# Kernel optimization log

Hardware: AMD Instinct MI355X
Metric: run time of the kernel (lower is better)

The kernel has to match this reference:

```python
import jax, jax.numpy as jnp
import numpy as np

B, S, D = 8, 1024, 1024
H, DH = 16, 64  # n_heads, d_head; D == H*DH


def setup_inputs() -> dict:
    key = jax.random.key(0)
    ks = jax.random.split(key, 7)
    scale = 1.0 / np.sqrt(DH)
    return {
        "images": jax.random.normal(ks[0], (B, S, D), dtype=jnp.float32),
        "Wq": jax.random.normal(ks[1], (H, DH, DH), dtype=jnp.float32) * scale,
        "bq": jax.random.normal(ks[2], (H, DH), dtype=jnp.float32) * scale,
        "Wk": jax.random.normal(ks[3], (H, DH, DH), dtype=jnp.float32) * scale,
        "bk": jax.random.normal(ks[4], (H, DH), dtype=jnp.float32) * scale,
        "Wv": jax.random.normal(ks[5], (H, DH, DH), dtype=jnp.float32) * scale,
        "bv": jax.random.normal(ks[6], (H, DH), dtype=jnp.float32) * scale,
    }


def reference(images, Wq, bq, Wk, bk, Wv, bv):
    Bn, Sn, Dn = images.shape
    x = images.reshape(Bn, Sn, H, DH)  # split hidden dim into per-head slices
    # torch Linear: y = x @ W.T + b, per head -> einsum over input dim d
    q = jnp.einsum("bshd,hod->bsho", x, Wq) + bq  # [B,S,H,DH]
    k = jnp.einsum("bshd,hod->bsho", x, Wk) + bk
    v = jnp.einsum("bshd,hod->bsho", x, Wv) + bv
    scores = jnp.einsum("bqhd,bkhd->bhqk", q, k) / jnp.sqrt(jnp.asarray(DH, x.dtype))
    attn = jax.nn.softmax(scores, axis=-1)  # [B,H,S,S]
    out = jnp.einsum("bhqk,bkhd->bqhd", attn, v)  # [B,S,H,DH]
    return out.reshape(Bn, Sn, Dn)  # hstack across heads == reshape back
```

## Files before the change

kernel.cpp:

```cpp
#include <hip/hip_runtime.h>
#include <hip/hip_bf16.h>

#define B_ 8
#define S_ 1024
#define D_ 1024
#define H_ 16
#define DH_ 64

typedef __attribute__((ext_vector_type(8))) short short8;
typedef __attribute__((ext_vector_type(8))) unsigned short ushort8;
typedef __attribute__((ext_vector_type(4))) unsigned short us4;
typedef __attribute__((ext_vector_type(4))) unsigned int uint4v;
typedef __attribute__((ext_vector_type(4))) float f32x4;

#define QSCALE 0.18033688011112042f

static __device__ __forceinline__ unsigned short f2bf(float f) {
    union { float f; unsigned u; } v; v.f = f;
    unsigned r = v.u + 0x7fffu + ((v.u >> 16) & 1u);
    return (unsigned short)(r >> 16);
}

static __device__ __forceinline__ void stage8(const float* __restrict__ src, unsigned short* dst) {
    float4 a = *reinterpret_cast<const float4*>(src);
    float4 b = *reinterpret_cast<const float4*>(src + 4);
    ushort8 r;
    r[0] = f2bf(a.x); r[1] = f2bf(a.y); r[2] = f2bf(a.z); r[3] = f2bf(a.w);
    r[4] = f2bf(b.x); r[5] = f2bf(b.y); r[6] = f2bf(b.z); r[7] = f2bf(b.w);
    *reinterpret_cast<ushort8*>(dst) = r;
}

static __device__ __forceinline__ unsigned int cvtpk(float a, float b) {
    unsigned int r;
    asm("v_cvt_pk_bf16_f32 %0, %1, %2" : "=v"(r) : "v"(a), "v"(b));
    return r;
}

__global__ __launch_bounds__(256) void qkv_proj(
    const float* __restrict__ x,
    const float* __restrict__ Wq, const float* __restrict__ bq,
    const float* __restrict__ Wk, const float* __restrict__ bk,
    const float* __restrict__ Wv, const float* __restrict__ bv,
    unsigned short* __restrict__ qo, unsigned short* __restrict__ ko,
    unsigned short* __restrict__ vo)
{
    const int bid   = blockIdx.x;
    const int stile = bid & 15;
    const int h     = (bid >> 4) & (H_ - 1);
    const int b     = bid >> 8;
    const int tid   = threadIdx.x;
    const int lane  = tid & 63;
    const int wave  = tid >> 6;
    const int lr    = lane & 15;
    const int lk    = lane >> 4;

    __shared__ __align__(16) unsigned short xs[64][72];
    __shared__ __align__(16) unsigned short wsh[3][64][72];

    {
        int row = tid >> 2;
        int col = (tid & 3) * 16;
        const float* src = x + ((size_t)(b * S_ + stile * 64 + row)) * D_ + h * DH_ + col;
        stage8(src,     &xs[row][col]);
        stage8(src + 8, &xs[row][col + 8]);
        const float* wsrc[3] = { Wq + h * DH_ * DH_, Wk + h * DH_ * DH_, Wv + h * DH_ * DH_ };
        #pragma unroll
        for (int p = 0; p < 3; ++p) {
            const float* s = wsrc[p] + row * DH_ + col;
            stage8(s,     &wsh[p][row][col]);
            stage8(s + 8, &wsh[p][row][col + 8]);
        }
    }
    __syncthreads();

    short8 a[2];
    #pragma unroll
    for (int kk = 0; kk < 2; ++kk)
        a[kk] = *reinterpret_cast<const short8*>(&xs[wave * 16 + lr][8 * lk + 32 * kk]);

    f32x4 acc[3][4];
    #pragma unroll
    for (int p = 0; p < 3; ++p)
        #pragma unroll
        for (int n = 0; n < 4; ++n)
            acc[p][n] = (f32x4){0.f, 0.f, 0.f, 0.f};

    #pragma unroll
    for (int p = 0; p < 3; ++p)
        #pragma unroll
        for (int kk = 0; kk < 2; ++kk)
            #pragma unroll
            for (int n = 0; n < 4; ++n) {
                short8 bf = *reinterpret_cast<const short8*>(&wsh[p][lr + 16 * n][8 * lk + 32 * kk]);
                acc[p][n] = __builtin_amdgcn_mfma_f32_16x16x32_bf16(a[kk], bf, acc[p][n], 0, 0, 0);
            }

    size_t base = ((size_t)(b * H_ + h) * S_ + stile * 64 + wave * 16) * DH_;
    #pragma unroll
    for (int p = 0; p < 2; ++p) {
        const float* bias = p ? (bk + h * DH_) : (bq + h * DH_);
        unsigned short* op = p ? ko : qo;
        #pragma unroll
        for (int n = 0; n < 4; ++n) {
            int col = lr + 16 * n;
            float bb = bias[col];
            #pragma unroll
            for (int r = 0; r < 4; ++r) {
                float val = acc[p][n][r] + bb;
                if (p == 0) val *= QSCALE;
                op[base + (size_t)(4 * lk + r) * DH_ + col] = f2bf(val);
            }
        }
    }
    {
        size_t vbase = (size_t)(b * H_ + h) * DH_ * S_;
        int s0 = stile * 64 + wave * 16 + 4 * lk;
        #pragma unroll
        for (int n = 0; n < 4; ++n) {
            int dh = lr + 16 * n;
            float bb = bv[h * DH_ + dh];
            us4 w;
            #pragma unroll
            for (int r = 0; r < 4; ++r) w[r] = f2bf(acc[2][n][r] + bb);
            *reinterpret_cast<us4*>(vo + vbase + (size_t)dh * S_ + s0) = w;
        }
    }
}

__global__ __launch_bounds__(256, 4) void attn_fwd(
    const unsigned short* __restrict__ q,
    const unsigned short* __restrict__ k,
    const unsigned short* __restrict__ vt,
    float* __restrict__ out)
{
    const int bid   = (blockIdx.x & 7) * 256 + (blockIdx.x >> 3);
    const int qtile = bid & 15;
    const int h     = (bid >> 4) & (H_ - 1);
    const int b     = bid >> 8;
    const int tid   = threadIdx.x;
    const int lane  = tid & 63;
    const int wave  = tid >> 6;
    const int lr    = lane & 15;
    const int lk    = lane >> 4;

    __shared__ __align__(16) unsigned short ks[2][64][72];
    __shared__ __align__(16) unsigned short vs[2][64][72];

    const size_t bh = (size_t)(b * H_ + h) * S_ * DH_;

    short8 qf[2];
    {
        const unsigned short* qp = q + bh + (size_t)(qtile * 64 + wave * 16 + lr) * DH_;
        #pragma unroll
        for (int kk = 0; kk < 2; ++kk)
            qf[kk] = *reinterpret_cast<const short8*>(qp + 8 * lk + 32 * kk);
    }

    const int srow = tid >> 2;
    const int scol = (tid & 3) * 16;
    const int prow = (srow & 0x23) | ((srow & 4) << 2) | ((srow & 0x18) >> 1);
    ushort8 kreg[2], vreg[2];

    {
        const unsigned short* srck = k + bh + (size_t)srow * DH_ + scol;
        kreg[0] = *reinterpret_cast<const ushort8*>(srck);
        kreg[1] = *reinterpret_cast<const ushort8*>(srck + 8);
        const unsigned short* srcv = vt + bh + (size_t)srow * S_ + scol;
        vreg[0] = *reinterpret_cast<const ushort8*>(srcv);
        vreg[1] = *reinterpret_cast<const ushort8*>(srcv + 8);
        *reinterpret_cast<ushort8*>(&ks[0][prow][scol])     = kreg[0];
        *reinterpret_cast<ushort8*>(&ks[0][prow][scol + 8]) = kreg[1];
        *reinterpret_cast<ushort8*>(&vs[0][srow][scol])     = vreg[0];
        *reinterpret_cast<ushort8*>(&vs[0][srow][scol + 8]) = vreg[1];
    }

    f32x4 acc[4];
    #pragma unroll
    for (int n = 0; n < 4; ++n) acc[n] = (f32x4){0.f, 0.f, 0.f, 0.f};
    float l = 0.f;

    const int NT = S_ / 64;
    for (int t = 0; t < NT; ++t) {
        __syncthreads();

        if (t + 1 < NT) {
            const unsigned short* srck = k + bh + (size_t)((t + 1) * 64 + srow) * DH_ + scol;
            kreg[0] = *reinterpret_cast<const ushort8*>(srck);
            kreg[1] = *reinterpret_cast<const ushort8*>(srck + 8);
            const unsigned short* srcv = vt + bh + (size_t)srow * S_ + (t + 1) * 64 + scol;
            vreg[0] = *reinterpret_cast<const ushort8*>(srcv);
            vreg[1] = *reinterpret_cast<const ushort8*>(srcv + 8);
        }
        const int cur = t & 1;

        f32x4 st[4];
        #pragma unroll
        for (int n = 0; n < 4; ++n) st[n] = (f32x4){0.f, 0.f, 0.f, 0.f};
        #pragma unroll
        for (int kk = 0; kk < 2; ++kk)
            #pragma unroll
            for (int n = 0; n < 4; ++n) {
                short8 ka = *reinterpret_cast<const short8*>(&ks[cur][16 * n + lr][8 * lk + 32 * kk]);
                st[n] = __builtin_amdgcn_mfma_f32_16x16x32_bf16(ka, qf[kk], st[n], 0, 0, 0);
            }

        #pragma unroll
        for (int n = 0; n < 4; ++n)
            #pragma unroll
            for (int r = 0; r < 4; ++r)
                st[n][r] = __builtin_amdgcn_exp2f(st[n][r]);
        float s01 = (st[0][0] + st[0][1]) + (st[0][2] + st[0][3]);
        float s23 = (st[1][0] + st[1][1]) + (st[1][2] + st[1][3]);
        float s45 = (st[2][0] + st[2][1]) + (st[2][2] + st[2][3]);
        float s67 = (st[3][0] + st[3][1]) + (st[3][2] + st[3][3]);
        l += (s01 + s23) + (s45 + s67);

        short8 pa[2];
        #pragma unroll
        for (int kk = 0; kk < 2; ++kk) {
            uint4v w4;
            w4[0] = cvtpk(st[2 * kk][0],     st[2 * kk][1]);
            w4[1] = cvtpk(st[2 * kk][2],     st[2 * kk][3]);
            w4[2] = cvtpk(st[2 * kk + 1][0], st[2 * kk + 1][1]);
            w4[3] = cvtpk(st[2 * kk + 1][2], st[2 * kk + 1][3]);
            pa[kk] = __builtin_bit_cast(short8, w4);
        }

        #pragma unroll
        for (int kk = 0; kk < 2; ++kk)
            #pragma unroll
            for (int n = 0; n < 4; ++n) {
                short8 va = *reinterpret_cast<const short8*>(&vs[cur][16 * n + lr][8 * lk + 32 * kk]);
                acc[n] = __builtin_amdgcn_mfma_f32_16x16x32_bf16(va, pa[kk], acc[n], 0, 0, 0);
            }

        if (t + 1 < NT) {
            const int nxt = cur ^ 1;
            *reinterpret_cast<ushort8*>(&ks[nxt][prow][scol])     = kreg[0];
            *reinterpret_cast<ushort8*>(&ks[nxt][prow][scol + 8]) = kreg[1];
            *reinterpret_cast<ushort8*>(&vs[nxt][srow][scol])     = vreg[0];
            *reinterpret_cast<ushort8*>(&vs[nxt][srow][scol + 8]) = vreg[1];
        }
    }

    l += __shfl_xor(l, 16, 64);
    l += __shfl_xor(l, 32, 64);
    const float inv = 1.f / l;
    const int qrow = qtile * 64 + wave * 16 + lr;
    float* op = out + (size_t)(b * S_ + qrow) * D_ + h * DH_;
    #pragma unroll
    for (int n = 0; n < 4; ++n) {
        float4 o;
        o.x = acc[n][0] * inv; o.y = acc[n][1] * inv;
        o.z = acc[n][2] * inv; o.w = acc[n][3] * inv;
        *reinterpret_cast<float4*>(op + 16 * n + 4 * lk) = o;
    }
}

extern "C" void kernel_launch(void* const* d_in, const int* in_sizes, int n_in,
                              void* d_out, int out_size, void* d_ws, size_t ws_size,
                              hipStream_t stream) {
    const float* x  = (const float*)d_in[0];
    const float* Wq = (const float*)d_in[1];
    const float* bq = (const float*)d_in[2];
    const float* Wk = (const float*)d_in[3];
    const float* bk = (const float*)d_in[4];
    const float* Wv = (const float*)d_in[5];
    const float* bv = (const float*)d_in[6];
    float* out = (float*)d_out;

    unsigned short* qw = (unsigned short*)d_ws;
    size_t per = (size_t)B_ * H_ * S_ * DH_;
    unsigned short* kw = qw + per;
    unsigned short* vw = kw + per;

    dim3 grid(B_ * H_ * (S_ / 64));
    qkv_proj<<<grid, 256, 0, stream>>>(x, Wq, bq, Wk, bk, Wv, bv, qw, kw, vw);
    attn_fwd<<<grid, 256, 0, stream>>>(qw, kw, vw, out);
}
```

Baseline: 77.65 us.

## Double query rows per attention block and XOR-swizzle K/V shared memory

Each attention block now handles 128 query rows instead of 64, with each wave owning two 16-row groups, so every K/V tile loaded into LDS feeds twice as many MFMAs. This halves global K/V traffic and staging work per query. The padded LDS layout is replaced by an XOR swizzle on 8-element chunks to avoid bank conflicts without padding. In exchange, register pressure doubles for accumulators and scores, and the grid shrinks to 1024 blocks, which may reduce occupancy.

```diff
diff --git a/kernel.cpp b/kernel.cpp
--- a/kernel.cpp
+++ b/kernel.cpp
@@ -133,127 +133,153 @@
     const unsigned short* __restrict__ vt,
     float* __restrict__ out)
 {
-    const int bid   = (blockIdx.x & 7) * 256 + (blockIdx.x >> 3);
-    const int qtile = bid & 15;
-    const int h     = (bid >> 4) & (H_ - 1);
-    const int b     = bid >> 8;
+    const int bid   = (blockIdx.x & 7) * 128 + (blockIdx.x >> 3);
+    const int qtile = bid & 7;
+    const int h     = (bid >> 3) & (H_ - 1);
+    const int b     = bid >> 7;
     const int tid   = threadIdx.x;
     const int lane  = tid & 63;
     const int wave  = tid >> 6;
     const int lr    = lane & 15;
     const int lk    = lane >> 4;
 
-    __shared__ __align__(16) unsigned short ks[2][64][72];
-    __shared__ __align__(16) unsigned short vs[2][64][72];
+    __shared__ __align__(16) unsigned short ks[2][64][64];
+    __shared__ __align__(16) unsigned short vs[2][64][64];
 
     const size_t bh = (size_t)(b * H_ + h) * S_ * DH_;
 
-    short8 qf[2];
+    short8 qf[2][2];
+    #pragma unroll
+    for (int g = 0; g < 2; ++g) {
+        const unsigned short* qp = q + bh + (size_t)(qtile * 128 + wave * 32 + 16 * g + lr) * DH_;
+        #pragma unroll
+        for (int kk = 0; kk < 2; ++kk)
+            qf[g][kk] = *reinterpret_cast<const short8*>(qp + 8 * lk + 32 * kk);
+    }
+
+    const int srow = tid >> 2;
+    const int c0   = (tid & 3) * 2;
+    const int prow = (srow & 0x23) | ((srow & 4) << 2) | ((srow & 0x18) >> 1);
+    const int kx   = prow & 7, vx = srow & 7;
+    ushort8 kreg[2], vreg[2];
+
     {
-        const unsigned short* qp = q + bh + (size_t)(qtile * 64 + wave * 16 + lr) * DH_;
-        #pragma unroll
-        for (int kk = 0; kk < 2; ++kk)
-            qf[kk] = *reinterpret_cast<const short8*>(qp + 8 * lk + 32 * kk);
-    }
-
-    const int srow = tid >> 2;
-    const int scol = (tid & 3) * 16;
-    const int prow = (srow & 0x23) | ((srow & 4) << 2) | ((srow & 0x18) >> 1);
-    ushort8 kreg[2], vreg[2];
-
-    {
-        const unsigned short* srck = k + bh + (size_t)srow * DH_ + scol;
+        const unsigned short* srck = k + bh + (size_t)srow * DH_ + c0 * 8;
         kreg[0] = *reinterpret_cast<const ushort8*>(srck);
         kreg[1] = *reinterpret_cast<const ushort8*>(srck + 8);
-        const unsigned short* srcv = vt + bh + (size_t)srow * S_ + scol;
+        const unsigned short* srcv = vt + bh + (size_t)srow * S_ + c0 * 8;
         vreg[0] = *reinterpret_cast<const ushort8*>(srcv);
         vreg[1] = *reinterpret_cast<const ushort8*>(srcv + 8);
-        *reinterpret_cast<ushort8*>(&ks[0][prow][scol])     = kreg[0];
-        *reinterpret_cast<ushort8*>(&ks[0][prow][scol + 8]) = kreg[1];
-        *reinterpret_cast<ushort8*>(&vs[0][srow][scol])     = vreg[0];
-        *reinterpret_cast<ushort8*>(&vs[0][srow][scol + 8]) = vreg[1];
-    }
-
-    f32x4 acc[4];
-    #pragma unroll
-    for (int n = 0; n < 4; ++n) acc[n] = (f32x4){0.f, 0.f, 0.f, 0.f};
-    float l = 0.f;
-
+        *reinterpret_cast<ushort8*>(&ks[0][prow][(c0 ^ kx) * 8])       = kreg[0];
+        *reinterpret_cast<ushort8*>(&ks[0][prow][((c0 + 1) ^ kx) * 8]) = kreg[1];
+        *reinterpret_cast<ushort8*>(&vs[0][srow][(c0 ^ vx) * 8])       = vreg[0];
+        *reinterpret_cast<ushort8*>(&vs[0][srow][((c0 + 1) ^ vx) * 8]) = vreg[1];
+    }
+
+    f32x4 acc[2][4];
+    #pragma unroll
+    for (int g = 0; g < 2; ++g)
+        #pragma unroll
+        for (int n = 0; n < 4; ++n) acc[g][n] = (f32x4){0.f, 0.f, 0.f, 0.f};
+    float l0 = 0.f, l1 = 0.f;
+
+    const int rx = lr & 7;
     const int NT = S_ / 64;
     for (int t = 0; t < NT; ++t) {
         __syncthreads();
 
         if (t + 1 < NT) {
-            const unsigned short* srck = k + bh + (size_t)((t + 1) * 64 + srow) * DH_ + scol;
+            const unsigned short* srck = k + bh + (size_t)((t + 1) * 64 + srow) * DH_ + c0 * 8;
             kreg[0] = *reinterpret_cast<const ushort8*>(srck);
             kreg[1] = *reinterpret_cast<const ushort8*>(srck + 8);
-            const unsigned short* srcv = vt + bh + (size_t)srow * S_ + (t + 1) * 64 + scol;
+            const unsigned short* srcv = vt + bh + (size_t)srow * S_ + (t + 1) * 64 + c0 * 8;
             vreg[0] = *reinterpret_cast<const ushort8*>(srcv);
             vreg[1] = *reinterpret_cast<const ushort8*>(srcv + 8);
         }
         const int cur = t & 1;
 
-        f32x4 st[4];
-        #pragma unroll
-        for (int n = 0; n < 4; ++n) st[n] = (f32x4){0.f, 0.f, 0.f, 0.f};
+        f32x4 st[2][4];
+        #pragma unroll
+        for (int g = 0; g < 2; ++g)
+            #pragma unroll
+            for (int n = 0; n < 4; ++n) st[g][n] = (f32x4){0.f, 0.f, 0.f, 0.f};
         #pragma unroll
         for (int kk = 0; kk < 2; ++kk)
             #pragma unroll
             for (int n = 0; n < 4; ++n) {
-                short8 ka = *reinterpret_cast<const short8*>(&ks[cur][16 * n + lr][8 * lk + 32 * kk]);
-                st[n] = __builtin_amdgcn_mfma_f32_16x16x32_bf16(ka, qf[kk], st[n], 0, 0, 0);
-            }
-
-        #pragma unroll
-        for (int n = 0; n < 4; ++n)
-            #pragma unroll
-            for (int r = 0; r < 4; ++r)
-                st[n][r] = __builtin_amdgcn_exp2f(st[n][r]);
-        float s01 = (st[0][0] + st[0][1]) + (st[0][2] + st[0][3]);
-        float s23 = (st[1][0] + st[1][1]) + (st[1][2] + st[1][3]);
-        float s45 = (st[2][0] + st[2][1]) + (st[2][2] + st[2][3]);
-        float s67 = (st[3][0] + st[3][1]) + (st[3][2] + st[3][3]);
-        l += (s01 + s23) + (s45 + s67);
-
-        short8 pa[2];
-        #pragma unroll
-        for (int kk = 0; kk < 2; ++kk) {
-            uint4v w4;
-            w4[0] = cvtpk(st[2 * kk][0],     st[2 * kk][1]);
-            w4[1] = cvtpk(st[2 * kk][2],     st[2 * kk][3]);
-            w4[2] = cvtpk(st[2 * kk + 1][0], st[2 * kk + 1][1]);
-            w4[3] = cvtpk(st[2 * kk + 1][2], st[2 * kk + 1][3]);
-            pa[kk] = __builtin_bit_cast(short8, w4);
-        }
+                short8 ka = *reinterpret_cast<const short8*>(
+                    &ks[cur][16 * n + lr][((lk + 4 * kk) ^ rx) * 8]);
+                st[0][n] = __builtin_amdgcn_mfma_f32_16x16x32_bf16(ka, qf[0][kk], st[0][n], 0, 0, 0);
+                st[1][n] = __builtin_amdgcn_mfma_f32_16x16x32_bf16(ka, qf[1][kk], st[1][n], 0, 0, 0);
+            }
+
+        #pragma unroll
+        for (int g = 0; g < 2; ++g)
+            #pragma unroll
+            for (int n = 0; n < 4; ++n)
+                #pragma unroll
+                for (int r = 0; r < 4; ++r)
+                    st[g][n][r] = __builtin_amdgcn_exp2f(st[g][n][r]);
+        {
+            float a0 = (st[0][0][0] + st[0][0][1]) + (st[0][0][2] + st[0][0][3]);
+            float a1 = (st[0][1][0] + st[0][1][1]) + (st[0][1][2] + st[0][1][3]);
+            float a2 = (st[0][2][0] + st[0][2][1]) + (st[0][2][2] + st[0][2][3]);
+            float a3 = (st[0][3][0] + st[0][3][1]) + (st[0][3][2] + st[0][3][3]);
+            l0 += (a0 + a1) + (a2 + a3);
+            float b0 = (st[1][0][0] + st[1][0][1]) + (st[1][0][2] + st[1][0][3]);
+            float b1 = (st[1][1][0] + st[1][1][1]) + (st[1][1][2] + st[1][1][3]);
+            float b2 = (st[1][2][0] + st[1][2][1]) + (st[1][2][2] + st[1][2][3]);
+            float b3 = (st[1][3][0] + st[1][3][1]) + (st[1][3][2] + st[1][3][3]);
+            l1 += (b0 + b1) + (b2 + b3);
+        }
+
+        short8 pa[2][2];
+        #pragma unroll
+        for (int g = 0; g < 2; ++g)
+            #pragma unroll
+            for (int kk = 0; kk < 2; ++kk) {
+                uint4v w4;
+                w4[0] = cvtpk(st[g][2 * kk][0],     st[g][2 * kk][1]);
+                w4[1] = cvtpk(st[g][2 * kk][2],     st[g][2 * kk][3]);
+                w4[2] = cvtpk(st[g][2 * kk + 1][0], st[g][2 * kk + 1][1]);
+                w4[3] = cvtpk(st[g][2 * kk + 1][2], st[g][2 * kk + 1][3]);
+                pa[g][kk] = __builtin_bit_cast(short8, w4);
+            }
 
         #pragma unroll
         for (int kk = 0; kk < 2; ++kk)
             #pragma unroll
             for (int n = 0; n < 4; ++n) {
-                short8 va = *reinterpret_cast<const short8*>(&vs[cur][16 * n + lr][8 * lk + 32 * kk]);
-                acc[n] = __builtin_amdgcn_mfma_f32_16x16x32_bf16(va, pa[kk], acc[n], 0, 0, 0);
+                short8 va = *reinterpret_cast<const short8*>(
+                    &vs[cur][16 * n + lr][((lk + 4 * kk) ^ rx) * 8]);
+                acc[0][n] = __builtin_amdgcn_mfma_f32_16x16x32_bf16(va, pa[0][kk], acc[0][n], 0, 0, 0);
+                acc[1][n] = __builtin_amdgcn_mfma_f32_16x16x32_bf16(va, pa[1][kk], acc[1][n], 0, 0, 0);
             }
 
         if (t + 1 < NT) {
             const int nxt = cur ^ 1;
-            *reinterpret_cast<ushort8*>(&ks[nxt][prow][scol])     = kreg[0];
-            *reinterpret_cast<ushort8*>(&ks[nxt][prow][scol + 8]) = kreg[1];
-            *reinterpret_cast<ushort8*>(&vs[nxt][srow][scol])     = vreg[0];
-            *reinterpret_cast<ushort8*>(&vs[nxt][srow][scol + 8]) = vreg[1];
-        }
-    }
-
-    l += __shfl_xor(l, 16, 64);
-    l += __shfl_xor(l, 32, 64);
-    const float inv = 1.f / l;
-    const int qrow = qtile * 64 + wave * 16 + lr;
-    float* op = out + (size_t)(b * S_ + qrow) * D_ + h * DH_;
-    #pragma unroll
-    for (int n = 0; n < 4; ++n) {
-        float4 o;
-        o.x = acc[n][0] * inv; o.y = acc[n][1] * inv;
-        o.z = acc[n][2] * inv; o.w = acc[n][3] * inv;
-        *reinterpret_cast<float4*>(op + 16 * n + 4 * lk) = o;
+            *reinterpret_cast<ushort8*>(&ks[nxt][prow][(c0 ^ kx) * 8])       = kreg[0];
+            *reinterpret_cast<ushort8*>(&ks[nxt][prow][((c0 + 1) ^ kx) * 8]) = kreg[1];
+            *reinterpret_cast<ushort8*>(&vs[nxt][srow][(c0 ^ vx) * 8])       = vreg[0];
+            *reinterpret_cast<ushort8*>(&vs[nxt][srow][((c0 + 1) ^ vx) * 8]) = vreg[1];
+        }
+    }
+
+    l0 += __shfl_xor(l0, 16, 64); l0 += __shfl_xor(l0, 32, 64);
+    l1 += __shfl_xor(l1, 16, 64); l1 += __shfl_xor(l1, 32, 64);
+    const float inv0 = 1.f / l0, inv1 = 1.f / l1;
+    #pragma unroll
+    for (int g = 0; g < 2; ++g) {
+        const float inv = g ? inv1 : inv0;
+        const int qrow = qtile * 128 + wave * 32 + 16 * g + lr;
+        float* op = out + (size_t)(b * S_ + qrow) * D_ + h * DH_;
+        #pragma unroll
+        for (int n = 0; n < 4; ++n) {
+            float4 o;
+            o.x = acc[g][n][0] * inv; o.y = acc[g][n][1] * inv;
+            o.z = acc[g][n][2] * inv; o.w = acc[g][n][3] * inv;
+            *reinterpret_cast<float4*>(op + 16 * n + 4 * lk) = o;
+        }
     }
 }
 
@@ -274,7 +300,6 @@
     unsigned short* kw = qw + per;
     unsigned short* vw = kw + per;
 
-    dim3 grid(B_ * H_ * (S_ / 64));
-    qkv_proj<<<grid, 256, 0, stream>>>(x, Wq, bq, Wk, bk, Wv, bv, qw, kw, vw);
-    attn_fwd<<<grid, 256, 0, stream>>>(qw, kw, vw, out);
-}
+    qkv_proj<<<dim3(B_ * H_ * (S_ / 64)), 256, 0, stream>>>(x, Wq, bq, Wk, bk, Wv, bv, qw, kw, vw);
+    attn_fwd<<<dim3(B_ * H_ * (S_ / 128)), 256, 0, stream>>>(qw, kw, vw, out);
+}
```

After: 68.82 us. 1.13x faster.
